# Kernel tuning notes

Hardware: AMD Instinct MI355X
Metric: run time of the kernel (lower is better)

The kernel has to match this reference:

```python
import jax, jax.numpy as jnp
import numpy as np

R = 5                       # kernels_radius
D = 2 * R + 1               # kernels_diameter
KERNELS_DESC = [
    {"weight": 0.9, "xy": 6.0, "image": 0.1},
    {"weight": 0.1, "xy": 6.0},
]


def _unfold(t, r):
    """torch F.unfold with padding=r, stride=1 -> [N, C, D, D, H, W]."""
    N, C, H, W = t.shape
    d = 2 * r + 1
    tp = jnp.pad(t, ((0, 0), (0, 0), (r, r), (r, r)))
    # fixed small loop over D*D kernel offsets (121), not over data dims
    pats = jnp.stack(
        [tp[:, :, i:i + H, j:j + W] for i in range(d) for j in range(d)],
        axis=2,
    )
    return pats.reshape(N, C, d, d, H, W)


def reference(x, y_hat):
    N, _, H, W = x.shape
    dt = x.dtype
    # xy coordinate feature [N, 2, H, W]: (col index, row index)
    cols = jnp.broadcast_to(jnp.arange(W, dtype=dt)[None, :], (H, W))
    rows = jnp.broadcast_to(jnp.arange(H, dtype=dt)[:, None], (H, W))
    xy = jnp.broadcast_to(jnp.stack([cols, rows], 0)[None], (N, 2, H, W))

    kernels = jnp.zeros((N, 1, D, D, H, W), dtype=dt)
    for desc in KERNELS_DESC:
        feats = []
        for modality, sigma in desc.items():
            if modality == 'weight':
                continue
            f = xy if modality == 'xy' else x
            feats.append(f / sigma)
        features = jnp.concatenate(feats, axis=1)          # [N, c, H, W]
        k = _unfold(features, R)                           # [N, c, D, D, H, W]
        k = k - k[:, :, R, R][:, :, None, None]            # diff to window center
        k = jnp.exp((-0.5 * k ** 2).sum(axis=1, keepdims=True))
        k = k.at[:, :, R, R].set(0.0)                      # zero self-affinity
        kernels = kernels + desc['weight'] * k

    Cy = y_hat.shape[1]
    yu = _unfold(y_hat, R)                                  # [N, Cy, D, D, H, W]
    prod = (kernels * yu).reshape(N, Cy, D * D, H, W).sum(axis=2)
    loss = kernels.sum() - (prod * y_hat).sum()
    denom = jnp.asarray(N * H * W, dtype=dt)
    return loss / denom


def setup_inputs() -> dict:
    key = jax.random.key(0)
    k1, k2 = jax.random.split(key)
    x = jax.random.normal(k1, (4, 3, 128, 128), dtype=jnp.float32)
    y_hat = jax.random.uniform(k2, (4, 21, 128, 128), dtype=jnp.float32)
    return {"x": x, "y_hat": y_hat}
```

## Files before the change

kernel.cpp:

```cpp
#include <hip/hip_runtime.h>

constexpr int IMG_H = 128;
constexpr int IMG_W = 128;
constexpr int N_IMG = 4;
constexpr int CXCH = 3;
constexpr int CYCH = 21;
constexpr int RAD = 5;
constexpr int DIA = 11;
constexpr int TILE_H = 8;
constexpr int TILE_W = 16;
constexpr int PT_H = TILE_H + 2 * RAD;
constexpr int PT_W = TILE_W + 2 * RAD;
constexpr int NPIX = PT_H * PT_W;
constexpr int PSTR = 28;
constexpr int NWAVES = 6;
constexpr int NTHREADS = NWAVES * 64;
constexpr int HW = IMG_H * IMG_W;

__device__ __forceinline__ float pair_term(
    const float* __restrict__ yc, const float* __restrict__ xc,
    const float4 q0, const float4 q1, const float4 q2,
    const float4 q3, const float4 q4, const float4 q5, float e1) {
    float dot = q5.x * yc[20];
    dot += q0.x * yc[0]  + q0.y * yc[1]  + q0.z * yc[2]  + q0.w * yc[3];
    dot += q1.x * yc[4]  + q1.y * yc[5]  + q1.z * yc[6]  + q1.w * yc[7];
    dot += q2.x * yc[8]  + q2.y * yc[9]  + q2.z * yc[10] + q2.w * yc[11];
    dot += q3.x * yc[12] + q3.y * yc[13] + q3.z * yc[14] + q3.w * yc[15];
    dot += q4.x * yc[16] + q4.y * yc[17] + q4.z * yc[18] + q4.w * yc[19];
    float d0 = q5.y - xc[0], d1 = q5.z - xc[1], d2 = q5.w - xc[2];
    float s2 = d0 * d0 + d1 * d1 + d2 * d2;
    float kv = e1 * (0.9f * __expf(-50.0f * s2) + 0.1f);
    return kv * (1.0f - dot);
}

__global__ __launch_bounds__(NTHREADS, 3)
void gcrf_kernel(const float* __restrict__ x, const float* __restrict__ y,
                 float* __restrict__ out) {
    __shared__ __align__(16) float s[NPIX * PSTR];
    __shared__ float s_red[NWAVES];

    const int tid = threadIdx.x;
    const int n = blockIdx.z;
    const int h0 = blockIdx.y * TILE_H;
    const int w0 = blockIdx.x * TILE_W;

    const float* xb = x + (size_t)n * CXCH * HW;
    const float* yb = y + (size_t)n * CYCH * HW;

    for (int p = tid; p < NPIX; p += NTHREADS) {
        int ti = p / PT_W, tj = p - ti * PT_W;
        int gh = h0 + ti - RAD, gw = w0 + tj - RAD;
        bool inb = ((unsigned)gh < (unsigned)IMG_H) &&
                   ((unsigned)gw < (unsigned)IMG_W);
        int gofs = gh * IMG_W + gw;
        float v[CYCH];
        #pragma unroll
        for (int c = 0; c < CYCH; c++) v[c] = inb ? yb[c * HW + gofs] : 0.0f;
        float xv[CXCH];
        #pragma unroll
        for (int c = 0; c < CXCH; c++) xv[c] = inb ? xb[c * HW + gofs] : 0.0f;
        float* d = &s[p * PSTR];
        #pragma unroll
        for (int q = 0; q < 5; q++)
            *(float4*)&d[q * 4] = make_float4(v[q * 4 + 0], v[q * 4 + 1],
                                              v[q * 4 + 2], v[q * 4 + 3]);
        *(float4*)&d[20] = make_float4(v[20], xv[0], xv[1], xv[2]);
    }
    __syncthreads();

    const int g = tid >> 6;
    const int lane = tid & 63;
    const int row = lane >> 3;
    const int cs = lane & 7;
    const int h = h0 + row;
    const int wA = w0 + cs * 2;
    const int cp = (row + RAD) * PT_W + (cs * 2 + RAD);

    float ycA[CYCH], ycB[CYCH], xcA[CXCH], xcB[CXCH];
    {
        const float* a = &s[cp * PSTR];
        const float* b = a + PSTR;
        #pragma unroll
        for (int q = 0; q < 5; q++) {
            float4 t = *(const float4*)&a[q * 4];
            ycA[q * 4 + 0] = t.x; ycA[q * 4 + 1] = t.y;
            ycA[q * 4 + 2] = t.z; ycA[q * 4 + 3] = t.w;
            float4 u = *(const float4*)&b[q * 4];
            ycB[q * 4 + 0] = u.x; ycB[q * 4 + 1] = u.y;
            ycB[q * 4 + 2] = u.z; ycB[q * 4 + 3] = u.w;
        }
        float4 t = *(const float4*)&a[20];
        ycA[20] = t.x; xcA[0] = t.y; xcA[1] = t.z; xcA[2] = t.w;
        float4 u = *(const float4*)&b[20];
        ycB[20] = u.x; xcB[0] = u.y; xcB[1] = u.z; xcB[2] = u.w;
    }

    const int di = g;
    const bool rowok = (h + di) < IMG_H;
    const float erow = __expf(-(float)(di * di) * (1.0f / 72.0f));
    const float EDJ[6] = {1.0f, 0.98620695f, 0.94595945f,
                          0.88249690f, 0.80073744f, 0.70664826f};

    float acco = 0.0f;
    float accp = 0.0f;

    if (g == 0) {
        #pragma unroll
        for (int i = 0; i < 2; i++) {
            int ww = wA + i;
            const float* xc = i ? xcB : xcA;
            int i0 = max(0, RAD - h), i1 = min(DIA - 1, IMG_H - 1 - h + RAD);
            int j0 = max(0, RAD - ww), j1 = min(DIA - 1, IMG_W - 1 - ww + RAD);
            int n_oob = DIA * DIA - (i1 - i0 + 1) * (j1 - j0 + 1);
            if (n_oob > 0) {
                float oxy = (float)(h * h + ww * ww) * (1.0f / 36.0f);
                float s2c = xc[0] * xc[0] + xc[1] * xc[1] + xc[2] * xc[2];
                float kvo = __expf(-0.5f * oxy) *
                            (0.9f * __expf(-50.0f * s2c) + 0.1f);
                acco += (float)n_oob * kvo;
            }
        }
        #pragma unroll
        for (int j = 6; j < 12; j++) {
            const float* nb = &s[(cp + (j - 5)) * PSTR];
            float4 q0 = *(const float4*)&nb[0];
            float4 q1 = *(const float4*)&nb[4];
            float4 q2 = *(const float4*)&nb[8];
            float4 q3 = *(const float4*)&nb[12];
            float4 q4 = *(const float4*)&nb[16];
            float4 q5 = *(const float4*)&nb[20];
            int gc = wA + (j - 5);
            float f = ((unsigned)gc < (unsigned)IMG_W) ? 1.0f : 0.0f;
            if (j <= 10)
                accp += pair_term(ycA, xcA, q0, q1, q2, q3, q4, q5,
                                  f * EDJ[j - 5]);
            if (j >= 7)
                accp += pair_term(ycB, xcB, q0, q1, q2, q3, q4, q5,
                                  f * EDJ[j - 6]);
        }
    } else {
        #pragma unroll
        for (int j = 0; j < 12; j++) {
            const float* nb = &s[(cp + di * PT_W + (j - 5)) * PSTR];
            float4 q0 = *(const float4*)&nb[0];
            float4 q1 = *(const float4*)&nb[4];
            float4 q2 = *(const float4*)&nb[8];
            float4 q3 = *(const float4*)&nb[12];
            float4 q4 = *(const float4*)&nb[16];
            float4 q5 = *(const float4*)&nb[20];
            int gc = wA + (j - 5);
            float f = (rowok && (unsigned)gc < (unsigned)IMG_W) ? erow : 0.0f;
            if (j <= 10) {
                int a = j >= 5 ? j - 5 : 5 - j;
                accp += pair_term(ycA, xcA, q0, q1, q2, q3, q4, q5, f * EDJ[a]);
            }
            if (j >= 1) {
                int a = j >= 6 ? j - 6 : 6 - j;
                accp += pair_term(ycB, xcB, q0, q1, q2, q3, q4, q5, f * EDJ[a]);
            }
        }
    }

    float total = acco + 2.0f * accp;

    #pragma unroll
    for (int sft = 32; sft > 0; sft >>= 1)
        total += __shfl_down(total, sft, 64);
    if (lane == 0) s_red[g] = total;
    __syncthreads();
    if (tid == 0) {
        float bs = 0.0f;
        #pragma unroll
        for (int wv = 0; wv < NWAVES; wv++) bs += s_red[wv];
        atomicAdd(out, bs * (1.0f / (float)(N_IMG * HW)));
    }
}

extern "C" void kernel_launch(void* const* d_in, const int* in_sizes, int n_in,
                              void* d_out, int out_size, void* d_ws, size_t ws_size,
                              hipStream_t stream) {
    const float* x = (const float*)d_in[0];
    const float* y = (const float*)d_in[1];
    float* out = (float*)d_out;
    hipMemsetAsync(out, 0, sizeof(float), stream);
    dim3 grid(IMG_W / TILE_W, IMG_H / TILE_H, N_IMG);
    gcrf_kernel<<<grid, NTHREADS, 0, stream>>>(x, y, out);
}
```

Baseline: 79.00 us.

## Split each row-offset wave's neighbor work across two waves

Doubles the block from 6 to 12 waves. Each vertical offset is now handled by two waves, one taking the left half of the column neighbors and one taking the right half, so each wave does about half as much pair work. The di=0 wave pair keeps the out-of-bounds correction on one wave and the right-side neighbors on the other. The halo load becomes a single guarded pass, since the block now has more threads than halo pixels. The aim is more latency hiding and a shorter critical path per block, at the cost of a larger block. The higher launch-bounds occupancy target may force tighter register limits or spills.

After: 113.4 us. 1.44x slower.

```diff
diff --git a/kernel.cpp b/kernel.cpp
--- a/kernel.cpp
+++ b/kernel.cpp
@@ -13,7 +13,7 @@
 constexpr int PT_W = TILE_W + 2 * RAD;
 constexpr int NPIX = PT_H * PT_W;
 constexpr int PSTR = 28;
-constexpr int NWAVES = 6;
+constexpr int NWAVES = 12;
 constexpr int NTHREADS = NWAVES * 64;
 constexpr int HW = IMG_H * IMG_W;
 
@@ -33,7 +33,15 @@
     return kv * (1.0f - dot);
 }
 
-__global__ __launch_bounds__(NTHREADS, 3)
+#define LOADQ(nb)                              \
+    float4 q0 = *(const float4*)&(nb)[0];      \
+    float4 q1 = *(const float4*)&(nb)[4];      \
+    float4 q2 = *(const float4*)&(nb)[8];      \
+    float4 q3 = *(const float4*)&(nb)[12];     \
+    float4 q4 = *(const float4*)&(nb)[16];     \
+    float4 q5 = *(const float4*)&(nb)[20];
+
+__global__ __launch_bounds__(NTHREADS, 6)
 void gcrf_kernel(const float* __restrict__ x, const float* __restrict__ y,
                  float* __restrict__ out) {
     __shared__ __align__(16) float s[NPIX * PSTR];
@@ -47,7 +55,8 @@
     const float* xb = x + (size_t)n * CXCH * HW;
     const float* yb = y + (size_t)n * CYCH * HW;
 
-    for (int p = tid; p < NPIX; p += NTHREADS) {
+    if (tid < NPIX) {
+        int p = tid;
         int ti = p / PT_W, tj = p - ti * PT_W;
         int gh = h0 + ti - RAD, gw = w0 + tj - RAD;
         bool inb = ((unsigned)gh < (unsigned)IMG_H) &&
@@ -70,11 +79,13 @@
 
     const int g = tid >> 6;
     const int lane = tid & 63;
+    const int di = g >> 1;
+    const int hh = g & 1;
     const int row = lane >> 3;
     const int cs = lane & 7;
     const int h = h0 + row;
-    const int wA = w0 + cs * 2;
-    const int cp = (row + RAD) * PT_W + (cs * 2 + RAD);
+    const int wA = w0 + 2 * cs;
+    const int cp = (row + RAD) * PT_W + (2 * cs + RAD);
 
     float ycA[CYCH], ycB[CYCH], xcA[CXCH], xcB[CXCH];
     {
@@ -95,11 +106,10 @@
         ycB[20] = u.x; xcB[0] = u.y; xcB[1] = u.z; xcB[2] = u.w;
     }
 
-    const int di = g;
     const bool rowok = (h + di) < IMG_H;
     const float erow = __expf(-(float)(di * di) * (1.0f / 72.0f));
-    const float EDJ[6] = {1.0f, 0.98620695f, 0.94595945f,
-                          0.88249690f, 0.80073744f, 0.70664826f};
+    constexpr float EDJ[6] = {1.0f, 0.98620695f, 0.94595945f,
+                              0.88249690f, 0.80073744f, 0.70664826f};
 
     float acco = 0.0f;
     float accp = 0.0f;
@@ -120,44 +130,32 @@
                 acco += (float)n_oob * kvo;
             }
         }
+    } else if (hh == 0) {
         #pragma unroll
-        for (int j = 6; j < 12; j++) {
-            const float* nb = &s[(cp + (j - 5)) * PSTR];
-            float4 q0 = *(const float4*)&nb[0];
-            float4 q1 = *(const float4*)&nb[4];
-            float4 q2 = *(const float4*)&nb[8];
-            float4 q3 = *(const float4*)&nb[12];
-            float4 q4 = *(const float4*)&nb[16];
-            float4 q5 = *(const float4*)&nb[20];
-            int gc = wA + (j - 5);
-            float f = ((unsigned)gc < (unsigned)IMG_W) ? 1.0f : 0.0f;
-            if (j <= 10)
-                accp += pair_term(ycA, xcA, q0, q1, q2, q3, q4, q5,
-                                  f * EDJ[j - 5]);
-            if (j >= 7)
+        for (int t = 0; t < 6; t++) {
+            const float* nb = &s[(cp + di * PT_W + (t - 5)) * PSTR];
+            LOADQ(nb);
+            int gc = wA + (t - 5);
+            float f = (rowok && (unsigned)gc < (unsigned)IMG_W) ? erow : 0.0f;
+            accp += pair_term(ycA, xcA, q0, q1, q2, q3, q4, q5, f * EDJ[5 - t]);
+            if (t >= 1)
                 accp += pair_term(ycB, xcB, q0, q1, q2, q3, q4, q5,
-                                  f * EDJ[j - 6]);
+                                  f * EDJ[6 - t]);
         }
     } else {
         #pragma unroll
-        for (int j = 0; j < 12; j++) {
-            const float* nb = &s[(cp + di * PT_W + (j - 5)) * PSTR];
-            float4 q0 = *(const float4*)&nb[0];
-            float4 q1 = *(const float4*)&nb[4];
-            float4 q2 = *(const float4*)&nb[8];
-            float4 q3 = *(const float4*)&nb[12];
-            float4 q4 = *(const float4*)&nb[16];
-            float4 q5 = *(const float4*)&nb[20];
-            int gc = wA + (j - 5);
+        for (int t = 0; t < 6; t++) {
+            const float* nb = &s[(cp + di * PT_W + (t + 1)) * PSTR];
+            LOADQ(nb);
+            int gc = wA + t + 1;
             float f = (rowok && (unsigned)gc < (unsigned)IMG_W) ? erow : 0.0f;
-            if (j <= 10) {
-                int a = j >= 5 ? j - 5 : 5 - j;
-                accp += pair_term(ycA, xcA, q0, q1, q2, q3, q4, q5, f * EDJ[a]);
-            }
-            if (j >= 1) {
-                int a = j >= 6 ? j - 6 : 6 - j;
-                accp += pair_term(ycB, xcB, q0, q1, q2, q3, q4, q5, f * EDJ[a]);
-            }
+            if (t <= 4)
+                accp += pair_term(ycA, xcA, q0, q1, q2, q3, q4, q5,
+                                  f * EDJ[t + 1]);
+            if (t >= 1)
+                accp += pair_term(ycB, xcB, q0, q1, q2, q3, q4, q5, f * EDJ[t]);
+            else if (di > 0)
+                accp += pair_term(ycB, xcB, q0, q1, q2, q3, q4, q5, f * EDJ[0]);
         }
     }
 
```
